# Performance work log

Measured on AMD Instinct MI355X. Metric: run time of the kernel, lower is better.

## Reference

```python
import jax, jax.numpy as jnp
import numpy as np

V, E, FF = 32000, 1024, 4096
T, B, S = 256, 8, 512
LN_EPS = 1e-5

def _ln(x, g, b):
    m = jnp.mean(x, -1, keepdims=True)
    v = jnp.var(x, -1, keepdims=True)
    return (x - m) * jax.lax.rsqrt(v + LN_EPS) * g + b

def setup_inputs() -> dict:
    key = jax.random.key(0)
    ks = jax.random.split(key, 16)
    inp = {
        "outs": jax.random.normal(ks[0], (T, B, E), jnp.float32),
        "mem": jax.random.normal(ks[1], (S, B, E), jnp.float32),
        "mem_bias": jax.random.normal(ks[2], (B, 1), jnp.float32),
        "in_proj_w": jax.random.normal(ks[3], (3 * E, E), jnp.float32) * 0.02,
        "in_proj_b": jnp.zeros((3 * E,), jnp.float32),
        "out_proj_w": jax.random.normal(ks[4], (E, E), jnp.float32) * 0.02,
        "out_proj_b": jnp.zeros((E,), jnp.float32),
        "aln_g": jnp.ones((E,), jnp.float32),
        "aln_b": jnp.zeros((E,), jnp.float32),
        "div_w": jax.random.normal(ks[5], (2, 2 * E), jnp.float32) * 0.02,
        "div_b": jnp.zeros((2,), jnp.float32),
        "fc1_w": jax.random.normal(ks[6], (FF, E), jnp.float32) * 0.02,
        "fc1_b": jnp.zeros((FF,), jnp.float32),
        "fc2_w": jax.random.normal(ks[7], (E, FF), jnp.float32) * 0.02,
        "fc2_b": jnp.zeros((E,), jnp.float32),
        "ffn_g": jnp.ones((E,), jnp.float32),
        "ffn_b": jnp.zeros((E,), jnp.float32),
        "vocab_w": jax.random.normal(ks[8], (V, E), jnp.float32) * 0.02,
        "mem_mask": jnp.ones((S, B), bool),
        "copy_seq": jax.random.randint(ks[9], (S, B), 0, V),
    }
    return inp

def reference(outs, mem, mem_bias, in_proj_w, in_proj_b, out_proj_w, out_proj_b,
              aln_g, aln_b, div_w, div_b, fc1_w, fc1_b, fc2_w, fc2_b,
              ffn_g, ffn_b, vocab_w, mem_mask, copy_seq):
    t, b, e = outs.shape
    s = mem.shape[0]
    # single-head alignment attention (eval mode: dropout is a no-op)
    q = (outs @ in_proj_w[:e].T + in_proj_b[:e]) * (e ** -0.5)  # [T,B,E]
    k = mem @ in_proj_w[e:2 * e].T + in_proj_b[e:2 * e]          # [S,B,E]
    v = mem @ in_proj_w[2 * e:].T + in_proj_b[2 * e:]            # [S,B,E]
    w = jnp.einsum('tbe,sbe->bts', q, k) + mem_bias[:, None, :]  # [B,T,S]
    keep = mem_mask.T[:, None, :]                                # [B,1,S]
    w = jnp.where(keep, w, -jnp.inf)
    w = jax.nn.softmax(w, axis=-1)                               # [B,T,S]
    attn = jnp.einsum('bts,sbe->tbe', w, v) @ out_proj_w.T + out_proj_b
    alignment = jnp.transpose(w, (1, 0, 2))                      # [T,B,S]
    # gates
    attn_norm = _ln(attn, aln_g, aln_b)
    gates = jax.nn.softmax(jnp.concatenate([outs, attn_norm], -1) @ div_w.T + div_b, -1)
    gen_gate, copy_gate = gates[..., :1], gates[..., 1:]
    # residual + FFN
    h = _ln(outs + attn, aln_g, aln_b)
    h = jax.nn.relu(h @ fc1_w.T + fc1_b) @ fc2_w.T + fc2_b
    h = _ln(h, ffn_g, ffn_b)
    # vocab distribution + copy scatter-add
    probs = gen_gate * jax.nn.softmax(h @ vocab_w.T, -1)         # [T,B,V]
    index = jnp.broadcast_to(copy_seq.T[None], (t, b, s))        # [T,B,S]
    copy_probs = copy_gate * alignment                           # [T,B,S]
    ti = jnp.arange(t)[:, None, None]
    bi = jnp.arange(b)[None, :, None]
    probs = probs.at[ti, bi, index].add(copy_probs)
    return jnp.log(probs + 1e-12)
```

## Files before the change

### kernel.cpp

```cpp
#include <hip/hip_runtime.h>
#include <math.h>

#define T_ 256
#define B_ 8
#define S_ 512
#define E_ 1024
#define FF_ 4096
#define V_ 32000
#define LN_EPSF 1e-5f

typedef __attribute__((ext_vector_type(8))) short short8;
typedef __attribute__((ext_vector_type(4))) float f32x4;
typedef unsigned short us;

__device__ __forceinline__ float blkSum(float v, float* sh) {
#pragma unroll
  for (int o = 32; o > 0; o >>= 1) v += __shfl_down(v, o, 64);
  if ((threadIdx.x & 63) == 0) sh[threadIdx.x >> 6] = v;
  __syncthreads();
  float r = sh[0] + sh[1] + sh[2] + sh[3];
  __syncthreads();
  return r;
}
__device__ __forceinline__ float blkMax(float v, float* sh) {
#pragma unroll
  for (int o = 32; o > 0; o >>= 1) v = fmaxf(v, __shfl_down(v, o, 64));
  if ((threadIdx.x & 63) == 0) sh[threadIdx.x >> 6] = v;
  __syncthreads();
  float r = fmaxf(fmaxf(sh[0], sh[1]), fmaxf(sh[2], sh[3]));
  __syncthreads();
  return r;
}
__device__ __forceinline__ float blkSum16(float v, float* sh) {
#pragma unroll
  for (int o = 32; o > 0; o >>= 1) v += __shfl_down(v, o, 64);
  if ((threadIdx.x & 63) == 0) sh[threadIdx.x >> 6] = v;
  __syncthreads();
  float r = 0.f;
#pragma unroll
  for (int i = 0; i < 16; ++i) r += sh[i];
  __syncthreads();
  return r;
}
__device__ __forceinline__ float blkMax16(float v, float* sh) {
#pragma unroll
  for (int o = 32; o > 0; o >>= 1) v = fmaxf(v, __shfl_down(v, o, 64));
  if ((threadIdx.x & 63) == 0) sh[threadIdx.x >> 6] = v;
  __syncthreads();
  float r = -INFINITY;
#pragma unroll
  for (int i = 0; i < 16; ++i) r = fmaxf(r, sh[i]);
  __syncthreads();
  return r;
}

__device__ __forceinline__ unsigned pkbf(float a, float b) {
  unsigned r;
  asm("v_cvt_pk_bf16_f32 %0, %1, %2" : "=v"(r) : "v"(a), "v"(b));
  return r;
}
__device__ __forceinline__ us bf16o(float a) {
  return (us)(pkbf(a, a) & 0xffffu);
}
__device__ __forceinline__ float bf2f(us u) {
  return __uint_as_float(((unsigned)u) << 16);
}

__device__ __forceinline__ void gl16(const us* g, us* l) {
  __builtin_amdgcn_global_load_lds(
      (const __attribute__((address_space(1))) void*)g,
      (__attribute__((address_space(3))) void*)l, 16, 0, 0);
}

__device__ __forceinline__ int swz(int idx) {
  return idx ^ (((idx >> 10) & 3) << 4);
}

__device__ __forceinline__ void tile_map(int& rowT, int& colT) {
  const unsigned nwg = gridDim.x * gridDim.y;
  const unsigned lin = blockIdx.y * gridDim.x + blockIdx.x;
  const unsigned nq = nwg >> 3, rr = nwg & 7;
  const unsigned xcd = lin & 7, idx = lin >> 3;
  const unsigned s =
      (xcd < rr ? xcd * (nq + 1) : rr * (nq + 1) + (xcd - rr) * nq) + idx;
  rowT = s % gridDim.x;
  colT = s / gridDim.x;
}

__global__ __launch_bounds__(256) void cvt_bf16(
    const float* __restrict__ in, us* __restrict__ o, int n4)
{
  int i = blockIdx.x * 256 + threadIdx.x;
  if (i < n4) {
    float4 f = ((const float4*)in)[i];
    ((uint2*)o)[i] = make_uint2(pkbf(f.x, f.y), pkbf(f.z, f.w));
  }
}

__global__ __launch_bounds__(256) void cvt_all(
    const float* __restrict__ s0, us* __restrict__ d0,
    const float* __restrict__ s1, us* __restrict__ d1,
    const float* __restrict__ s2, us* __restrict__ d2,
    const float* __restrict__ s3, us* __restrict__ d3,
    const float* __restrict__ s4, us* __restrict__ d4,
    const float* __restrict__ s5, us* __restrict__ d5)
{
  int j = blockIdx.x * 256 + threadIdx.x;
  const float* s; us* d;
  if (j < 524288) { s = s0; d = d0; }
  else { j -= 524288; if (j < 1048576) { s = s1; d = d1; }
  else { j -= 1048576; if (j < 786432) { s = s2; d = d2; }
  else { j -= 786432; if (j < 262144) { s = s3; d = d3; }
  else { j -= 262144; if (j < 1048576) { s = s4; d = d4; }
  else { j -= 1048576; if (j >= 1048576) return; s = s5; d = d5; } } } } }
  float4 f = ((const float4*)s)[j];
  ((uint2*)d)[j] = make_uint2(pkbf(f.x, f.y), pkbf(f.z, f.w));
}

template<int CBF>
__global__ __launch_bounds__(512) void gemm_8p(
    const us* __restrict__ A, const us* __restrict__ Bm,
    const float* __restrict__ bias, void* __restrict__ Cv,
    int K, int lda, int ldb, int ldc, float scale, int relu)
{
  __shared__ us sA[2][16384], sB[2][16384];
  int rowT, colT;
  tile_map(rowT, colT);
  const int row0 = rowT * 256, col0 = colT * 256;
  const us* Ap = A + (long)row0 * lda;
  const us* Bp = Bm + (long)col0 * ldb;

  const int lane = threadIdx.x & 63, wid = threadIdx.x >> 6;
  const int wr = wid >> 2, wc = wid & 3;
  const int lr = lane & 15, kb = lane >> 4;

  long asrc[4], bsrc[4];
  int dst[4];
#pragma unroll
  for (int i = 0; i < 4; ++i) {
    int c = wid * 4 + i;
    int kg = c & 7, rq = c >> 3;
    asrc[i] = (long)(rq * 64 + lane) * lda + kg * 8;
    bsrc[i] = (long)(rq * 64 + lane) * ldb + kg * 8;
    dst[i] = kg * 2048 + rq * 512;
  }

  f32x4 acc[8][4];
#pragma unroll
  for (int j = 0; j < 8; ++j)
#pragma unroll
    for (int ni = 0; ni < 4; ++ni) {
      f32x4 z = {0.f, 0.f, 0.f, 0.f};
      acc[j][ni] = z;
    }

  const int nt = K >> 6;
#pragma unroll
  for (int i = 0; i < 4; ++i) gl16(Bp + bsrc[i], &sB[0][dst[i]]);
#pragma unroll
  for (int i = 0; i < 4; ++i) gl16(Ap + asrc[i], &sA[0][dst[i]]);
  asm volatile("s_waitcnt vmcnt(0)" ::: "memory");
  __builtin_amdgcn_s_barrier();

  for (int t = 0; t < nt; ++t) {
    const int buf = t & 1, nbuf = buf ^ 1;
    const long kN = (long)(t + 1) << 6;
    const bool pf = (t + 1) < nt;
    short8 bfr[4], af[4];

#pragma unroll
    for (int ni = 0; ni < 4; ++ni)
      bfr[ni] = *(const short8*)&sB[buf][kb * 2048 + (wc * 64 + ni * 16 + lr) * 8];
#pragma unroll
    for (int mi = 0; mi < 4; ++mi)
      af[mi] = *(const short8*)&sA[buf][kb * 2048 + (wr * 128 + mi * 16 + lr) * 8];
    if (pf) {
#pragma unroll
      for (int i = 0; i < 4; ++i) gl16(Bp + bsrc[i] + kN, &sB[nbuf][dst[i]]);
    }
    __builtin_amdgcn_s_barrier();
    asm volatile("s_waitcnt lgkmcnt(0)" ::: "memory");
    __builtin_amdgcn_sched_barrier(0);
    __builtin_amdgcn_s_setprio(1);
#pragma unroll
    for (int mi = 0; mi < 4; ++mi)
#pragma unroll
      for (int ni = 0; ni < 4; ++ni)
        acc[mi][ni] = __builtin_amdgcn_mfma_f32_16x16x32_bf16(
            af[mi], bfr[ni], acc[mi][ni], 0, 0, 0);
    __builtin_amdgcn_s_setprio(0);
    __builtin_amdgcn_s_barrier();

#pragma unroll
    for (int mi = 0; mi < 4; ++mi)
      af[mi] = *(const short8*)&sA[buf][kb * 2048 + (wr * 128 + 64 + mi * 16 + lr) * 8];
    if (pf) {
#pragma unroll
      for (int i = 0; i < 4; ++i) gl16(Ap + asrc[i] + kN, &sA[nbuf][dst[i]]);
    }
    __builtin_amdgcn_s_barrier();
    asm volatile("s_waitcnt lgkmcnt(0)" ::: "memory");
    __builtin_amdgcn_sched_barrier(0);
    __builtin_amdgcn_s_setprio(1);
#pragma unroll
    for (int mi = 0; mi < 4; ++mi)
#pragma unroll
      for (int ni = 0; ni < 4; ++ni)
        acc[4 + mi][ni] = __builtin_amdgcn_mfma_f32_16x16x32_bf16(
            af[mi], bfr[ni], acc[4 + mi][ni], 0, 0, 0);
    __builtin_amdgcn_s_setprio(0);
    __builtin_amdgcn_s_barrier();

#pragma unroll
    for (int ni = 0; ni < 4; ++ni)
      bfr[ni] = *(const short8*)&sB[buf][(4 + kb) * 2048 + (wc * 64 + ni * 16 + lr) * 8];
#pragma unroll
    for (int mi = 0; mi < 4; ++mi)
      af[mi] = *(const short8*)&sA[buf][(4 + kb) * 2048 + (wr * 128 + mi * 16 + lr) * 8];
    __builtin_amdgcn_s_barrier();
    asm volatile("s_waitcnt lgkmcnt(0)" ::: "memory");
    __builtin_amdgcn_sched_barrier(0);
    __builtin_amdgcn_s_setprio(1);
#pragma unroll
    for (int mi = 0; mi < 4; ++mi)
#pragma unroll
      for (int ni = 0; ni < 4; ++ni)
        acc[mi][ni] = __builtin_amdgcn_mfma_f32_16x16x32_bf16(
            af[mi], bfr[ni], acc[mi][ni], 0, 0, 0);
    __builtin_amdgcn_s_setprio(0);
    __builtin_amdgcn_s_barrier();

#pragma unroll
    for (int mi = 0; mi < 4; ++mi)
      af[mi] = *(const short8*)&sA[buf][(4 + kb) * 2048 + (wr * 128 + 64 + mi * 16 + lr) * 8];
    __builtin_amdgcn_s_barrier();
    asm volatile("s_waitcnt lgkmcnt(0)" ::: "memory");
    __builtin_amdgcn_sched_barrier(0);
    __builtin_amdgcn_s_setprio(1);
#pragma unroll
    for (int mi = 0; mi < 4; ++mi)
#pragma unroll
      for (int ni = 0; ni < 4; ++ni)
        acc[4 + mi][ni] = __builtin_amdgcn_mfma_f32_16x16x32_bf16(
            af[mi], bfr[ni], acc[4 + mi][ni], 0, 0, 0);
    __builtin_amdgcn_s_setprio(0);
    asm volatile("s_waitcnt vmcnt(0)" ::: "memory");
    __builtin_amdgcn_s_barrier();
  }

#pragma unroll
  for (int j = 0; j < 8; ++j)
#pragma unroll
    for (int ni = 0; ni < 4; ++ni) {
      int col = col0 + wc * 64 + ni * 16 + lr;
      float bv = bias ? bias[col] : 0.0f;
#pragma unroll
      for (int r = 0; r < 4; ++r) {
        int row = row0 + wr * 128 + (j >> 2) * 64 + (j & 3) * 16 + kb * 4 + r;
        float vv = (acc[j][ni][r] + bv) * scale;
        if (relu) vv = fmaxf(vv, 0.0f);
        if constexpr (CBF)
          ((us*)Cv)[(long)row * ldc + col] = bf16o(vv);
        else
          ((float*)Cv)[(long)row * ldc + col] = vv;
      }
    }
}

template<int CBF>
__global__ __launch_bounds__(256) void gemm_gl(
    const us* __restrict__ A, const us* __restrict__ Bm,
    const float* __restrict__ bias, const float* __restrict__ sbias,
    void* __restrict__ Cv, int K, int lda, int ldb, int ldc,
    long aB, long bB, long cB, float scale, int relu)
{
  __shared__ us sA[3][4096], sB[3][4096];
  int rowT, colT;
  tile_map(rowT, colT);
  const int bz = blockIdx.z;
  const int row0 = rowT * 128, col0 = colT * 128;
  const us* Ap = A + (long)bz * aB + (long)row0 * lda;
  const us* Bp = Bm + (long)bz * bB + (long)col0 * ldb;
  const float sb = sbias ? sbias[bz] : 0.0f;

  const int lane = threadIdx.x & 63, wid = threadIdx.x >> 6;
  const int wr = wid >> 1, wc = wid & 1;
  const int lr = lane & 15, kb = lane >> 4;

  const int r1 = threadIdx.x & 127, q1 = threadIdx.x >> 7;
  const long a1 = (long)r1 * lda + q1 * 8, a2 = a1 + 16;
  const long b1 = (long)r1 * ldb + q1 * 8, b2 = b1 + 16;
  const int dof1 = wid * 512, dof2 = 2048 + wid * 512;

  f32x4 acc[4][4];
#pragma unroll
  for (int mi = 0; mi < 4; ++mi)
#pragma unroll
    for (int ni = 0; ni < 4; ++ni) {
      f32x4 z = {0.f, 0.f, 0.f, 0.f};
      acc[mi][ni] = z;
    }

  auto stage = [&](int buf, long k0) {
    gl16(Ap + a1 + k0, &sA[buf][dof1]);
    gl16(Ap + a2 + k0, &sA[buf][dof2]);
    gl16(Bp + b1 + k0, &sB[buf][dof1]);
    gl16(Bp + b2 + k0, &sB[buf][dof2]);
  };
  auto compute = [&](int buf) {
    short8 af[4], bfr[4];
#pragma unroll
    for (int mi = 0; mi < 4; ++mi)
      af[mi] = *(const short8*)&sA[buf][kb * 1024 + (wr * 64 + mi * 16 + lr) * 8];
#pragma unroll
    for (int ni = 0; ni < 4; ++ni)
      bfr[ni] = *(const short8*)&sB[buf][kb * 1024 + (wc * 64 + ni * 16 + lr) * 8];
#pragma unroll
    for (int mi = 0; mi < 4; ++mi)
#pragma unroll
      for (int ni = 0; ni < 4; ++ni)
        acc[mi][ni] = __builtin_amdgcn_mfma_f32_16x16x32_bf16(
            af[mi], bfr[ni], acc[mi][ni], 0, 0, 0);
  };

  const int nt = K >> 5;
  stage(0, 0);
  stage(1, 32);
  stage(2, 64);
  for (int t = 0; t < nt; ++t) {
    if (t + 2 < nt)      asm volatile("s_waitcnt vmcnt(8)" ::: "memory");
    else if (t + 1 < nt) asm volatile("s_waitcnt vmcnt(4)" ::: "memory");
    else                 asm volatile("s_waitcnt vmcnt(0)" ::: "memory");
    __builtin_amdgcn_s_barrier();
    const int buf = t % 3;
    compute(buf);
    __builtin_amdgcn_s_barrier();
    if (t + 3 < nt) stage(buf, (long)(t + 3) << 5);
  }

  char* Cbase = (char*)Cv + (long)bz * cB * (CBF ? 2 : 4);
#pragma unroll
  for (int mi = 0; mi < 4; ++mi)
#pragma unroll
    for (int ni = 0; ni < 4; ++ni) {
      int col = col0 + wc * 64 + ni * 16 + lr;
      float bv = bias ? bias[col] : 0.0f;
#pragma unroll
      for (int r = 0; r < 4; ++r) {
        int row = row0 + wr * 64 + mi * 16 + kb * 4 + r;
        float vv = (acc[mi][ni][r] + bv) * scale + sb;
        if (relu) vv = fmaxf(vv, 0.0f);
        if constexpr (CBF)
          ((us*)Cbase)[(long)row * ldc + col] = bf16o(vv);
        else
          ((float*)Cbase)[(long)row * ldc + col] = vv;
      }
    }
}

__global__ __launch_bounds__(256) void gemm_nt_bb(
    const us* __restrict__ A, const us* __restrict__ Bm,
    us* __restrict__ C, int K, int lda, int ldb, int ldc,
    long aB, long bB, long cB)
{
  __shared__ us sA[4096];
  __shared__ us sB[4096];
  int rowT, colT;
  tile_map(rowT, colT);
  const int bz = blockIdx.z;
  const int row0 = rowT * 128, col0 = colT * 128;
  const us* Ap = A + (long)bz * aB + (long)row0 * lda;
  const us* Bp = Bm + (long)bz * bB + col0;

  const int lane = threadIdx.x & 63, wid = threadIdx.x >> 6;
  const int wr = wid >> 1, wc = wid & 1;
  const int lr = lane & 15, kb = lane >> 4;
  const int kq = threadIdx.x & 7, m0 = threadIdx.x >> 3;
  const int k8 = threadIdx.x >> 5, c4 = threadIdx.x & 31;

  f32x4 acc[4][4];
#pragma unroll
  for (int mi = 0; mi < 4; ++mi)
#pragma unroll
    for (int ni = 0; ni < 4; ++ni) {
      f32x4 z = {0.f, 0.f, 0.f, 0.f};
      acc[mi][ni] = z;
    }

  uint2 ra[4], rb[4];
#pragma unroll
  for (int i = 0; i < 4; ++i) {
    int m = m0 + 32 * i;
    ra[i] = *(const uint2*)(Ap + (long)m * lda + kq * 4);
    int kk = k8 + 8 * i;
    rb[i] = *(const uint2*)(Bp + (long)kk * ldb + c4 * 4);
  }

  for (int k0 = 0;;) {
#pragma unroll
    for (int i = 0; i < 4; ++i) {
      int m = m0 + 32 * i;
      int idx = swz(((kq >> 1) * 128 + m) * 8 + (kq & 1) * 4);
      *(uint2*)&sA[idx] = ra[i];
      int b0 = (i * 128 + c4 * 4) * 8 + k8;
      sB[swz(b0)]      = (us)(rb[i].x & 0xffffu);
      sB[swz(b0 + 8)]  = (us)(rb[i].x >> 16);
      sB[swz(b0 + 16)] = (us)(rb[i].y & 0xffffu);
      sB[swz(b0 + 24)] = (us)(rb[i].y >> 16);
    }
    __syncthreads();
    k0 += 32;
    if (k0 < K) {
#pragma unroll
      for (int i = 0; i < 4; ++i) {
        int m = m0 + 32 * i;
        ra[i] = *(const uint2*)(Ap + (long)m * lda + k0 + kq * 4);
        int kk = k8 + 8 * i;
        rb[i] = *(const uint2*)(Bp + (long)(k0 + kk) * ldb + c4 * 4);
      }
    }
    short8 af[4], bfr[4];
#pragma unroll
    for (int mi = 0; mi < 4; ++mi)
      af[mi] = *(const short8*)&sA[swz((kb * 128 + wr * 64 + mi * 16 + lr) * 8)];
#pragma unroll
    for (int ni = 0; ni < 4; ++ni)
      bfr[ni] = *(const short8*)&sB[swz((kb * 128 + wc * 64 + ni * 16 + lr) * 8)];
#pragma unroll
    for (int mi = 0; mi < 4; ++mi)
#pragma unroll
      for (int ni = 0; ni < 4; ++ni)
        acc[mi][ni] = __builtin_amdgcn_mfma_f32_16x16x32_bf16(
            af[mi], bfr[ni], acc[mi][ni], 0, 0, 0);
    __syncthreads();
    if (k0 >= K) break;
  }

  us* Cp = C + (long)bz * cB;
#pragma unroll
  for (int mi = 0; mi < 4; ++mi)
#pragma unroll
    for (int ni = 0; ni < 4; ++ni) {
      int col = col0 + wc * 64 + ni * 16 + lr;
#pragma unroll
      for (int r = 0; r < 4; ++r) {
        int row = row0 + wr * 64 + mi * 16 + kb * 4 + r;
        Cp[(long)row * ldc + col] = bf16o(acc[mi][ni][r]);
      }
    }
}

__global__ __launch_bounds__(256) void attn_softmax(
    float* __restrict__ w, us* __restrict__ wbf, const int* __restrict__ mask)
{
  __shared__ float sh[4];
  const int blk = blockIdx.x;
  const int b = blk / T_;
  float* row = w + (long)blk * S_;
  us* rowb = wbf + (long)blk * S_;
  const int s0 = threadIdx.x, s1 = threadIdx.x + 256;
  const bool k0 = mask[s0 * B_ + b] != 0;
  const bool k1 = mask[s1 * B_ + b] != 0;
  float x0 = k0 ? row[s0] : -INFINITY;
  float x1 = k1 ? row[s1] : -INFINITY;
  float m = blkMax(fmaxf(x0, x1), sh);
  float e0 = k0 ? expf(x0 - m) : 0.0f;
  float e1 = k1 ? expf(x1 - m) : 0.0f;
  float sum = blkSum(e0 + e1, sh);
  float inv = sum > 0.0f ? 1.0f / sum : 0.0f;
  float p0 = e0 * inv, p1 = e1 * inv;
  row[s0] = p0; row[s1] = p1;
  rowb[s0] = bf16o(p0); rowb[s1] = bf16o(p1);
}

__global__ __launch_bounds__(256) void gates_h1(
    const float* __restrict__ outs, const float* __restrict__ attn,
    const float* __restrict__ aln_g, const float* __restrict__ aln_b,
    const float* __restrict__ div_w, const float* __restrict__ div_b,
    us* __restrict__ h1, float* __restrict__ gen, float* __restrict__ cpy)
{
  __shared__ float sh[4];
  const long base = (long)blockIdx.x * E_;
  float a[4], o[4];
  float sa = 0.f, sa2 = 0.f, shh = 0.f, sh2 = 0.f;
#pragma unroll
  for (int i = 0; i < 4; ++i) {
    int e = threadIdx.x + 256 * i;
    a[i] = attn[base + e];
    o[i] = outs[base + e];
    sa += a[i]; sa2 += a[i] * a[i];
    float t = o[i] + a[i];
    shh += t; sh2 += t * t;
  }
  sa  = blkSum(sa, sh);
  sa2 = blkSum(sa2, sh);
  shh = blkSum(shh, sh);
  sh2 = blkSum(sh2, sh);
  const float ma = sa / E_, va = sa2 / E_ - ma * ma;
  const float mh = shh / E_, vh = sh2 / E_ - mh * mh;
  const float ra = rsqrtf(va + LN_EPSF), rh = rsqrtf(vh + LN_EPSF);

  float z0 = 0.f, z1 = 0.f;
#pragma unroll
  for (int i = 0; i < 4; ++i) {
    int e = threadIdx.x + 256 * i;
    float g = aln_g[e], bb = aln_b[e];
    float an = (a[i] - ma) * ra * g + bb;
    float hv = (o[i] + a[i] - mh) * rh * g + bb;
    h1[base + e] = bf16o(hv);
    z0 += o[i] * div_w[e]          + an * div_w[E_ + e];
    z1 += o[i] * div_w[2 * E_ + e] + an * div_w[3 * E_ + e];
  }
  z0 = blkSum(z0, sh);
  z1 = blkSum(z1, sh);
  if (threadIdx.x == 0) {
    z0 += div_b[0]; z1 += div_b[1];
    float mm = fmaxf(z0, z1);
    float e0 = expf(z0 - mm), e1 = expf(z1 - mm);
    float inv = 1.0f / (e0 + e1);
    gen[blockIdx.x] = e0 * inv;
    cpy[blockIdx.x] = e1 * inv;
  }
}

__global__ __launch_bounds__(256) void ln_bf16(
    const float* __restrict__ x, const float* __restrict__ g,
    const float* __restrict__ b, us* __restrict__ o)
{
  __shared__ float sh[4];
  const long base = (long)blockIdx.x * E_;
  float v[4];
  float s = 0.f, s2 = 0.f;
#pragma unroll
  for (int i = 0; i < 4; ++i) {
    v[i] = x[base + threadIdx.x + 256 * i];
    s += v[i]; s2 += v[i] * v[i];
  }
  s  = blkSum(s, sh);
  s2 = blkSum(s2, sh);
  const float m = s / E_, var = s2 / E_ - m * m;
  const float r = rsqrtf(var + LN_EPSF);
#pragma unroll
  for (int i = 0; i < 4; ++i) {
    int e = threadIdx.x + 256 * i;
    o[base + e] = bf16o((v[i] - m) * r * g[e] + b[e]);
  }
}

__global__ __launch_bounds__(1024) void vocab_softmax_bf(
    float* __restrict__ out, const float* __restrict__ gen,
    const int* __restrict__ copy_seq)
{
  __shared__ float sh[16];
  __shared__ unsigned bits[1000];
  const int r = blockIdx.x, b = r & 7;
  const int tid = threadIdx.x;
  const short8* row8 = (const short8*)((us*)out + (long)r * 64000 + 32000);
  float4* row4 = (float4*)(out + (long)r * V_);

  if (tid < 1000) bits[tid] = 0u;
  __syncthreads();
  if (tid < S_) {
    int idx = copy_seq[tid * B_ + b];
    atomicOr(&bits[idx >> 5], 1u << (idx & 31));
  }

  float vals[32];
  float mx = -INFINITY;
#pragma unroll
  for (int i = 0; i < 4; ++i) {
    int f = tid + (i << 10);
    if (f < 4000) {
      short8 v8 = row8[f];
#pragma unroll
      for (int j = 0; j < 8; ++j) {
        float x = bf2f((us)v8[j]);
        vals[i * 8 + j] = x;
        mx = fmaxf(mx, x);
      }
    } else {
#pragma unroll
      for (int j = 0; j < 8; ++j) vals[i * 8 + j] = -INFINITY;
    }
  }
  const float gmx = blkMax16(mx, sh);

  float s = 0.f;
#pragma unroll
  for (int i = 0; i < 32; ++i) {
    vals[i] = expf(vals[i] - gmx);
    s += vals[i];
  }
  s = blkSum16(s, sh);

  const float scale = gen[r] / s;
#pragma unroll
  for (int i = 0; i < 4; ++i) {
    int f = tid + (i << 10);
    if (f < 4000) {
      int e0 = f * 8;
#pragma unroll
      for (int h = 0; h < 2; ++h) {
        float4 p;
        int eb = e0 + h * 4;
        p.x = vals[i * 8 + h * 4 + 0] * scale;
        p.y = vals[i * 8 + h * 4 + 1] * scale;
        p.z = vals[i * 8 + h * 4 + 2] * scale;
        p.w = vals[i * 8 + h * 4 + 3] * scale;
        p.x = (bits[eb >> 5] >> (eb & 31) & 1) ? p.x : logf(p.x + 1e-12f);
        p.y = (bits[(eb+1) >> 5] >> ((eb+1) & 31) & 1) ? p.y : logf(p.y + 1e-12f);
        p.z = (bits[(eb+2) >> 5] >> ((eb+2) & 31) & 1) ? p.z : logf(p.z + 1e-12f);
        p.w = (bits[(eb+3) >> 5] >> ((eb+3) & 31) & 1) ? p.w : logf(p.w + 1e-12f);
        row4[(e0 >> 2) + h] = p;
      }
    }
  }
}

__global__ __launch_bounds__(256) void scatter_k(
    float* __restrict__ out, const float* __restrict__ w,
    const float* __restrict__ cpy, const int* __restrict__ copy_seq)
{
  const int g = blockIdx.x * 256 + threadIdx.x;
  const int r = g >> 9, sdx = g & 511;
  const int t = r >> 3, b = r & 7;
  const float contrib = cpy[r] * w[((long)b * T_ + t) * S_ + sdx];
  atomicAdd(&out[(long)r * V_ + copy_seq[sdx * B_ + b]], contrib);
}

__global__ __launch_bounds__(1024) void fixup_log(
    float* __restrict__ out, const int* __restrict__ copy_seq)
{
  __shared__ unsigned bits[1000];
  const int r = blockIdx.x, b = r & 7;
  const int tid = threadIdx.x;
  float* row = out + (long)r * V_;
  if (tid < 1000) bits[tid] = 0u;
  __syncthreads();
  if (tid < S_) {
    int idx = copy_seq[tid * B_ + b];
    atomicOr(&bits[idx >> 5], 1u << (idx & 31));
  }
  __syncthreads();
  if (tid < 1000) {
    unsigned wd = bits[tid];
    while (wd) {
      int j = __ffs(wd) - 1;
      int idx = (tid << 5) + j;
      row[idx] = logf(row[idx] + 1e-12f);
      wd &= wd - 1;
    }
  }
}

extern "C" void kernel_launch(void* const* d_in, const int* in_sizes, int n_in,
                              void* d_out, int out_size, void* d_ws, size_t ws_size,
                              hipStream_t stream) {
  (void)in_sizes; (void)n_in; (void)out_size; (void)ws_size;
  const float* outs     = (const float*)d_in[0];
  const float* mem      = (const float*)d_in[1];
  const float* mem_bias = (const float*)d_in[2];
  const float* in_w     = (const float*)d_in[3];
  const float* in_b     = (const float*)d_in[4];
  const float* ow       = (const float*)d_in[5];
  const float* ob       = (const float*)d_in[6];
  const float* aln_g    = (const float*)d_in[7];
  const float* aln_b    = (const float*)d_in[8];
  const float* div_w    = (const float*)d_in[9];
  const float* div_b    = (const float*)d_in[10];
  const float* fc1_w    = (const float*)d_in[11];
  const float* fc1_b    = (const float*)d_in[12];
  const float* fc2_w    = (const float*)d_in[13];
  const float* fc2_b    = (const float*)d_in[14];
  const float* ffn_g    = (const float*)d_in[15];
  const float* ffn_b    = (const float*)d_in[16];
  const float* vocab_w  = (const float*)d_in[17];
  const int*   mask     = (const int*)d_in[18];
  const int*   copy_seq = (const int*)d_in[19];
  float* out = (float*)d_out;
  char*  wsb = (char*)d_ws;

  us* in_w_bf  = (us*)(wsb + 0);
  us* ow_bf    = (us*)(wsb + 6291456);
  us* fc1_bf   = (us*)(wsb + 8388608);
  us* fc2_bf   = (us*)(wsb + 16777216);
  us* outs_bf  = (us*)(wsb + 25165824);
  us* h1_bf    = outs_bf;
  us* mem_bf   = (us*)(wsb + 29360128);
  float* attn  = (float*)(wsb + 29360128);
  float* h2    = attn;
  us* q_bf     = (us*)(wsb + 37748736);
  us* kv_bf    = (us*)(wsb + 41943040);
  us* w_bf     = (us*)(wsb + 58720256);
  us* ctx_bf   = (us*)(wsb + 60817408);
  us* vocab_bf = (us*)(wsb + 0);
  float* w_    = (float*)(wsb + 65536000);
  us* h2_bf    = (us*)(wsb + 69730304);
  float* gen   = (float*)(wsb + 73924608);
  float* cpy   = gen + 2048;
  us* mid_bf   = (us*)d_out;
  us* logits   = (us*)d_out + 32000;

  dim3 blk(256), blk5(512);
  cvt_all<<<dim3(18432), blk, 0, stream>>>(
      outs, outs_bf, mem, mem_bf, in_w, in_w_bf, ow, ow_bf,
      fc1_w, fc1_bf, fc2_w, fc2_bf);
  gemm_gl<1><<<dim3(16, 8), blk, 0, stream>>>(outs_bf, in_w_bf, in_b, nullptr, q_bf,
      1024, 1024, 1024, 1024, 0, 0, 0, 0.03125f, 0);
  gemm_gl<1><<<dim3(32, 16), blk, 0, stream>>>(mem_bf, in_w_bf + E_ * E_, in_b + E_, nullptr, kv_bf,
      1024, 1024, 1024, 2048, 0, 0, 0, 1.0f, 0);
  gemm_gl<0><<<dim3(2, 4, 8), blk, 0, stream>>>(q_bf, kv_bf, nullptr, mem_bias, w_,
      1024, B_ * E_, B_ * 2048, S_, E_, 2048, (long)T_ * S_, 1.0f, 0);
  attn_softmax<<<dim3(B_ * T_), blk, 0, stream>>>(w_, w_bf, mask);
  gemm_nt_bb<<<dim3(2, 8, 8), blk, 0, stream>>>(w_bf, kv_bf + 1024, ctx_bf,
      512, S_, B_ * 2048, B_ * E_, (long)T_ * S_, 2048, E_);
  gemm_gl<0><<<dim3(16, 8), blk, 0, stream>>>(ctx_bf, ow_bf, ob, nullptr, attn,
      1024, 1024, 1024, 1024, 0, 0, 0, 1.0f, 0);
  gates_h1<<<dim3(2048), blk, 0, stream>>>(outs, attn, aln_g, aln_b, div_w, div_b,
      h1_bf, gen, cpy);
  gemm_gl<1><<<dim3(16, 32), blk, 0, stream>>>(h1_bf, fc1_bf, fc1_b, nullptr, mid_bf,
      1024, 1024, 1024, 4096, 0, 0, 0, 1.0f, 1);
  gemm_gl<0><<<dim3(16, 8), blk, 0, stream>>>(mid_bf, fc2_bf, fc2_b, nullptr, h2,
      4096, 4096, 4096, 1024, 0, 0, 0, 1.0f, 0);
  ln_bf16<<<dim3(2048), blk, 0, stream>>>(h2, ffn_g, ffn_b, h2_bf);
  cvt_bf16<<<dim3(32000), blk, 0, stream>>>(vocab_w, vocab_bf, 8192000);
  gemm_8p<1><<<dim3(8, 125), blk5, 0, stream>>>(h2_bf, vocab_bf, nullptr, logits,
      1024, 1024, 1024, 64000, 1.0f, 0);
  vocab_softmax_bf<<<dim3(2048), dim3(1024), 0, stream>>>(out, gen, copy_seq);
  scatter_k<<<dim3(4096), blk, 0, stream>>>(out, w_, cpy, copy_seq);
  fixup_log<<<dim3(2048), dim3(1024), 0, stream>>>(out, copy_seq);
}
```

Measured before the change: 769.8 us.

## Fuse copy scatter-add into vocab softmax and split-K the fc2 GEMM

The copy-probability scatter-add and the final log now happen inside the vocab softmax kernel. Each row's contributions are accumulated into a 32000-float shared-memory buffer, which removes the separate scatter and fixup kernels and a second read-modify-write pass over the output rows. Separately, the fc2 GEMM is split along K into two partial results, which the layernorm kernel sums together with the bias. This gives the fc2 GEMM more blocks, at the cost of writing and reading an extra partial buffer. The 128 KB shared buffer limits each CU to one 1024-thread block, so occupancy in the softmax kernel drops.

```diff
diff --git a/kernel.cpp b/kernel.cpp
--- a/kernel.cpp
+++ b/kernel.cpp
@@ -523,8 +523,9 @@
   }
 }
 
-__global__ __launch_bounds__(256) void ln_bf16(
-    const float* __restrict__ x, const float* __restrict__ g,
+__global__ __launch_bounds__(256) void ln2_bf16(
+    const float* __restrict__ x1, const float* __restrict__ x2,
+    const float* __restrict__ bias, const float* __restrict__ g,
     const float* __restrict__ b, us* __restrict__ o)
 {
   __shared__ float sh[4];
@@ -533,7 +534,8 @@
   float s = 0.f, s2 = 0.f;
 #pragma unroll
   for (int i = 0; i < 4; ++i) {
-    v[i] = x[base + threadIdx.x + 256 * i];
+    int e = threadIdx.x + 256 * i;
+    v[i] = x1[base + e] + x2[base + e] + bias[e];
     s += v[i]; s2 += v[i] * v[i];
   }
   s  = blkSum(s, sh);
@@ -547,22 +549,23 @@
   }
 }
 
-__global__ __launch_bounds__(1024) void vocab_softmax_bf(
+__global__ __launch_bounds__(1024) void vocab_final(
     float* __restrict__ out, const float* __restrict__ gen,
+    const float* __restrict__ cpy, const float* __restrict__ w,
     const int* __restrict__ copy_seq)
 {
+  __shared__ float scat[32000];
   __shared__ float sh[16];
-  __shared__ unsigned bits[1000];
-  const int r = blockIdx.x, b = r & 7;
+  const int r = blockIdx.x, b = r & 7, t = r >> 3;
   const int tid = threadIdx.x;
   const short8* row8 = (const short8*)((us*)out + (long)r * 64000 + 32000);
   float4* row4 = (float4*)(out + (long)r * V_);
 
-  if (tid < 1000) bits[tid] = 0u;
+  for (int i = tid; i < V_; i += 1024) scat[i] = 0.f;
   __syncthreads();
   if (tid < S_) {
-    int idx = copy_seq[tid * B_ + b];
-    atomicOr(&bits[idx >> 5], 1u << (idx & 31));
+    float contrib = cpy[r] * w[((long)b * T_ + t) * S_ + tid];
+    atomicAdd(&scat[copy_seq[tid * B_ + b]], contrib);
   }
 
   float vals[32];
@@ -603,52 +606,12 @@
       for (int h = 0; h < 2; ++h) {
         float4 p;
         int eb = e0 + h * 4;
-        p.x = vals[i * 8 + h * 4 + 0] * scale;
-        p.y = vals[i * 8 + h * 4 + 1] * scale;
-        p.z = vals[i * 8 + h * 4 + 2] * scale;
-        p.w = vals[i * 8 + h * 4 + 3] * scale;
-        p.x = (bits[eb >> 5] >> (eb & 31) & 1) ? p.x : logf(p.x + 1e-12f);
-        p.y = (bits[(eb+1) >> 5] >> ((eb+1) & 31) & 1) ? p.y : logf(p.y + 1e-12f);
-        p.z = (bits[(eb+2) >> 5] >> ((eb+2) & 31) & 1) ? p.z : logf(p.z + 1e-12f);
-        p.w = (bits[(eb+3) >> 5] >> ((eb+3) & 31) & 1) ? p.w : logf(p.w + 1e-12f);
+        p.x = logf(vals[i * 8 + h * 4 + 0] * scale + scat[eb + 0] + 1e-12f);
+        p.y = logf(vals[i * 8 + h * 4 + 1] * scale + scat[eb + 1] + 1e-12f);
+        p.z = logf(vals[i * 8 + h * 4 + 2] * scale + scat[eb + 2] + 1e-12f);
+        p.w = logf(vals[i * 8 + h * 4 + 3] * scale + scat[eb + 3] + 1e-12f);
         row4[(e0 >> 2) + h] = p;
       }
-    }
-  }
-}
-
-__global__ __launch_bounds__(256) void scatter_k(
-    float* __restrict__ out, const float* __restrict__ w,
-    const float* __restrict__ cpy, const int* __restrict__ copy_seq)
-{
-  const int g = blockIdx.x * 256 + threadIdx.x;
-  const int r = g >> 9, sdx = g & 511;
-  const int t = r >> 3, b = r & 7;
-  const float contrib = cpy[r] * w[((long)b * T_ + t) * S_ + sdx];
-  atomicAdd(&out[(long)r * V_ + copy_seq[sdx * B_ + b]], contrib);
-}
-
-__global__ __launch_bounds__(1024) void fixup_log(
-    float* __restrict__ out, const int* __restrict__ copy_seq)
-{
-  __shared__ unsigned bits[1000];
-  const int r = blockIdx.x, b = r & 7;
-  const int tid = threadIdx.x;
-  float* row = out + (long)r * V_;
-  if (tid < 1000) bits[tid] = 0u;
-  __syncthreads();
-  if (tid < S_) {
-    int idx = copy_seq[tid * B_ + b];
-    atomicOr(&bits[idx >> 5], 1u << (idx & 31));
-  }
-  __syncthreads();
-  if (tid < 1000) {
-    unsigned wd = bits[tid];
-    while (wd) {
-      int j = __ffs(wd) - 1;
-      int idx = (tid << 5) + j;
-      row[idx] = logf(row[idx] + 1e-12f);
-      wd &= wd - 1;
     }
   }
 }
@@ -683,12 +646,13 @@
   us* in_w_bf  = (us*)(wsb + 0);
   us* ow_bf    = (us*)(wsb + 6291456);
   us* fc1_bf   = (us*)(wsb + 8388608);
+  float* h2b   = (float*)(wsb + 8388608);
   us* fc2_bf   = (us*)(wsb + 16777216);
   us* outs_bf  = (us*)(wsb + 25165824);
   us* h1_bf    = outs_bf;
   us* mem_bf   = (us*)(wsb + 29360128);
   float* attn  = (float*)(wsb + 29360128);
-  float* h2    = attn;
+  float* h2a   = attn;
   us* q_bf     = (us*)(wsb + 37748736);
   us* kv_bf    = (us*)(wsb + 41943040);
   us* w_bf     = (us*)(wsb + 58720256);
@@ -720,13 +684,11 @@
       h1_bf, gen, cpy);
   gemm_gl<1><<<dim3(16, 32), blk, 0, stream>>>(h1_bf, fc1_bf, fc1_b, nullptr, mid_bf,
       1024, 1024, 1024, 4096, 0, 0, 0, 1.0f, 1);
-  gemm_gl<0><<<dim3(16, 8), blk, 0, stream>>>(mid_bf, fc2_bf, fc2_b, nullptr, h2,
-      4096, 4096, 4096, 1024, 0, 0, 0, 1.0f, 0);
-  ln_bf16<<<dim3(2048), blk, 0, stream>>>(h2, ffn_g, ffn_b, h2_bf);
+  gemm_gl<0><<<dim3(16, 8, 2), blk, 0, stream>>>(mid_bf, fc2_bf, nullptr, nullptr, h2a,
+      2048, 4096, 4096, 1024, 2048, 2048, (long)(h2b - h2a), 1.0f, 0);
+  ln2_bf16<<<dim3(2048), blk, 0, stream>>>(h2a, h2b, fc2_b, ffn_g, ffn_b, h2_bf);
   cvt_bf16<<<dim3(32000), blk, 0, stream>>>(vocab_w, vocab_bf, 8192000);
   gemm_8p<1><<<dim3(8, 125), blk5, 0, stream>>>(h2_bf, vocab_bf, nullptr, logits,
       1024, 1024, 1024, 64000, 1.0f, 0);
-  vocab_softmax_bf<<<dim3(2048), dim3(1024), 0, stream>>>(out, gen, copy_seq);
-  scatter_k<<<dim3(4096), blk, 0, stream>>>(out, w_, cpy, copy_seq);
-  fixup_log<<<dim3(2048), dim3(1024), 0, stream>>>(out, copy_seq);
-}
+  vocab_final<<<dim3(2048), dim3(1024), 0, stream>>>(out, gen, cpy, w_, copy_seq);
+}
```

New measurement: 667.3 us. 1.15x faster.
